# Optimization experiments

Hardware: AMD Instinct MI355X
Metric: run time of the kernel (lower is better)

## Reference

```python
import jax, jax.numpy as jnp
import numpy as np

EPS = 1e-12  # F.normalize default eps

def _l2norm(x, axis):
    n = jnp.sqrt(jnp.sum(x * x, axis=axis, keepdims=True))
    return x / jnp.maximum(n, EPS)

def setup_inputs() -> dict:
    key = jax.random.key(0)
    ks = jax.random.split(key, 6)
    N, C, K, B, OUT = 200000, 256, 64, 8, 1024
    alpha = 100.0
    feat = jax.random.normal(ks[0], (N, C), dtype=jnp.float32)
    batch_ids = jax.random.randint(ks[1], (N,), 0, B, dtype=jnp.int32)
    centroids = jax.random.uniform(ks[2], (K, C), dtype=jnp.float32)
    # _init_params: conv weight = 2*alpha*centroids, bias = -alpha*||centroid||_2
    conv_w = 2.0 * alpha * centroids
    conv_b = -alpha * jnp.sqrt(jnp.sum(centroids * centroids, axis=1))
    fc_w = jax.random.normal(ks[3], (OUT, K * C), dtype=jnp.float32) * (1.0 / np.sqrt(K * C))
    fc_b = jax.random.normal(ks[4], (OUT,), dtype=jnp.float32) * 0.01
    return {"feat": feat, "batch_ids": batch_ids, "centroids": centroids,
            "conv_w": conv_w, "conv_b": conv_b, "fc_w": fc_w, "fc_b": fc_b,
            "batch_size": B}

def reference(feat, batch_ids, centroids, conv_w, conv_b, fc_w, fc_b, batch_size):
    B = int(batch_size)
    K, C = centroids.shape
    # descriptor-wise L2 normalization (normalize_input=True)
    x = _l2norm(feat, axis=1)                       # [N, C]
    # 1x1 conv == linear: soft assignment logits per point
    logits = x @ conv_w.T + conv_b                  # [N, K]
    soft = jax.nn.softmax(logits, axis=1)           # [N, K]
    # Per-batch aggregation (replaces the python loop):
    # vlad[b,k,:] = sum_{p in b} soft[p,k] * x[p,:] - (sum_{p in b} soft[p,k]) * centroids[k,:]
    onehot = jax.nn.one_hot(batch_ids, B, dtype=x.dtype)          # [N, B]
    A = jnp.einsum('nb,nk,nc->bkc', onehot, soft, x)              # [B, K, C]
    S = jax.ops.segment_sum(soft, batch_ids, num_segments=B)      # [B, K]
    vlad = A - S[:, :, None] * centroids[None, :, :]              # [B, K, C]
    vlad = _l2norm(vlad, axis=2)                                  # intra-normalization over C
    v = vlad.reshape(B, K * C)
    out = v @ fc_w.T + fc_b                                       # [B, 1024]
    return _l2norm(out, axis=1)
```

## Files before the change

kernel.cpp:

```cpp
#include <hip/hip_runtime.h>
#include <hip/hip_bf16.h>

typedef __attribute__((ext_vector_type(8))) short bf16x8;
typedef __attribute__((ext_vector_type(4))) float f32x4;

#define PCAP 768

__global__ void p0_wsplit(const float* __restrict__ convw,
                          short* __restrict__ whi, short* __restrict__ wlo)
{
    int e = blockIdx.x * 256 + threadIdx.x;
    if (e >= 2048) return;
    int lane = e & 63;
    int kstep = (e >> 6) & 7;
    int nt = e >> 9;
    int cluster = nt * 16 + (lane & 15);
    int ch0 = kstep * 32 + (lane >> 4) * 8;
    const float* src = convw + cluster * 256 + ch0;
    #pragma unroll
    for (int j = 0; j < 8; ++j) {
        float x = src[j];
        unsigned u = __float_as_uint(x);
        unsigned uh = u & 0xffff0000u;
        float r = x - __uint_as_float(uh);
        whi[e * 8 + j] = (short)(u >> 16);
        wlo[e * 8 + j] = (short)(__float_as_uint(r) >> 16);
    }
}

__global__ __launch_bounds__(256) void p1_mfma(
    const float* __restrict__ feat, const int* __restrict__ bids,
    const short* __restrict__ whi, const short* __restrict__ wlo,
    const float* __restrict__ convb,
    float* __restrict__ soft, float* __restrict__ invn, int* __restrict__ cnts, int N)
{
    __shared__ float ssq_lds[64];
    __shared__ int cnt[8];
    const int t = threadIdx.x;
    if (t < 8) cnt[t] = 0;
    const int w = t >> 6, lane = t & 63;
    const int m = lane & 15, quad = lane >> 4;
    const int p0 = blockIdx.x * 64;
    const int gp = p0 + w * 16 + m;
    const bool valid = gp < N;

    f32x4 acc[4];
    #pragma unroll
    for (int nt = 0; nt < 4; ++nt) acc[nt] = (f32x4){0.f, 0.f, 0.f, 0.f};
    float ssq = 0.f;

    const float* frow = feat + (size_t)gp * 256 + quad * 8;
    const bf16x8* WH = (const bf16x8*)whi;
    const bf16x8* WL = (const bf16x8*)wlo;

    for (int ks = 0; ks < 8; ++ks) {
        float x[8];
        if (valid) {
            float4 v0 = *(const float4*)(frow + ks * 32);
            float4 v1 = *(const float4*)(frow + ks * 32 + 4);
            x[0] = v0.x; x[1] = v0.y; x[2] = v0.z; x[3] = v0.w;
            x[4] = v1.x; x[5] = v1.y; x[6] = v1.z; x[7] = v1.w;
        } else {
            #pragma unroll
            for (int j = 0; j < 8; ++j) x[j] = 0.f;
        }
        bf16x8 ahi, alo;
        #pragma unroll
        for (int j = 0; j < 8; ++j) {
            unsigned u = __float_as_uint(x[j]);
            unsigned uh = u & 0xffff0000u;
            float r = x[j] - __uint_as_float(uh);
            ahi[j] = (short)(u >> 16);
            alo[j] = (short)(__float_as_uint(r) >> 16);
            ssq += x[j] * x[j];
        }
        #pragma unroll
        for (int nt = 0; nt < 4; ++nt) {
            bf16x8 bhi = WH[(nt * 8 + ks) * 64 + lane];
            bf16x8 blo = WL[(nt * 8 + ks) * 64 + lane];
            acc[nt] = __builtin_amdgcn_mfma_f32_16x16x32_bf16(ahi, bhi, acc[nt], 0, 0, 0);
            acc[nt] = __builtin_amdgcn_mfma_f32_16x16x32_bf16(ahi, blo, acc[nt], 0, 0, 0);
            acc[nt] = __builtin_amdgcn_mfma_f32_16x16x32_bf16(alo, bhi, acc[nt], 0, 0, 0);
        }
    }

    ssq += __shfl_xor(ssq, 16);
    ssq += __shfl_xor(ssq, 32);
    if (quad == 0) ssq_lds[w * 16 + m] = ssq;
    __syncthreads();

    float bias[4];
    #pragma unroll
    for (int nt = 0; nt < 4; ++nt) bias[nt] = convb[nt * 16 + m];

    #pragma unroll
    for (int r = 0; r < 4; ++r) {
        int pl = quad * 4 + r;
        int gpt = p0 + w * 16 + pl;
        float inv = rsqrtf(fmaxf(ssq_lds[w * 16 + pl], 1e-24f));
        float v[4];
        #pragma unroll
        for (int nt = 0; nt < 4; ++nt) v[nt] = acc[nt][r] * inv + bias[nt];
        float mx = fmaxf(fmaxf(v[0], v[1]), fmaxf(v[2], v[3]));
        #pragma unroll
        for (int off = 8; off >= 1; off >>= 1) mx = fmaxf(mx, __shfl_xor(mx, off));
        float e[4];
        float s = 0.f;
        #pragma unroll
        for (int nt = 0; nt < 4; ++nt) { e[nt] = __expf(v[nt] - mx); s += e[nt]; }
        #pragma unroll
        for (int off = 8; off >= 1; off >>= 1) s += __shfl_xor(s, off);
        float rs = 1.0f / s;
        if (gpt < N) {
            #pragma unroll
            for (int nt = 0; nt < 4; ++nt)
                soft[(size_t)gpt * 64 + nt * 16 + m] = e[nt] * rs;
            if (m == 0) {
                invn[gpt] = inv;
                atomicAdd(&cnt[bids[gpt]], 1);
            }
        }
    }
    __syncthreads();
    if (t < 8) atomicAdd(&cnts[t], cnt[t]);
}

__global__ void p2_offsets(const int* __restrict__ cnts, int* __restrict__ offs, int* __restrict__ cur)
{
    if (threadIdx.x == 0) {
        int acc = 0;
        for (int b = 0; b < 8; ++b) { offs[b] = acc; cur[b] = acc; acc += cnts[b]; }
        offs[8] = acc;
    }
}

__global__ __launch_bounds__(256) void p2_scatter(
    const int* __restrict__ bids, int* __restrict__ cur, int* __restrict__ perm, int N)
{
    __shared__ int lcnt[8], lbase[8];
    const int t = threadIdx.x;
    if (t < 8) lcnt[t] = 0;
    __syncthreads();
    int p = blockIdx.x * 256 + t;
    int b = 0, my = 0;
    bool ok = p < N;
    if (ok) { b = bids[p]; my = atomicAdd(&lcnt[b], 1); }
    __syncthreads();
    if (t < 8) lbase[t] = atomicAdd(&cur[t], lcnt[t]);
    __syncthreads();
    if (ok) perm[lbase[b] + my] = p;
}

__global__ __launch_bounds__(256) void p3_mfma(
    const float* __restrict__ feat, const float* __restrict__ soft,
    const float* __restrict__ invn, const int* __restrict__ perm,
    const int* __restrict__ offs, float* __restrict__ partial,
    float* __restrict__ S, int split)
{
    __shared__ short xsT_hi[256 * 32];
    __shared__ short xsT_lo[256 * 32];
    __shared__ short sT_hi[64 * 32];
    __shared__ short sT_lo[64 * 32];
    __shared__ int   pidxL[PCAP];
    __shared__ float invL[PCAP];

    const int b  = blockIdx.x / split;
    const int sp = blockIdx.x % split;
    const int start = offs[b], end = offs[b + 1];
    const int len = end - start;
    const int chunk = (len + split - 1) / split;
    const int s0 = start + sp * chunk;
    int myLen = end - s0;
    myLen = max(0, min(myLen, chunk));
    myLen = min(myLen, PCAP);

    const int t = threadIdx.x;
    const int w = t >> 6, lane = t & 63;
    const int m = lane & 15, quad = lane >> 4;

    for (int i = t; i < myLen; i += 256) pidxL[i] = perm[s0 + i];
    __syncthreads();
    for (int i = t; i < myLen; i += 256) invL[i] = invn[pidxL[i]];
    __syncthreads();

    f32x4 acc[16];
    #pragma unroll
    for (int ct = 0; ct < 16; ++ct) acc[ct] = (f32x4){0.f, 0.f, 0.f, 0.f};
    float sacc = 0.f;

    const int nch = (myLen + 31) >> 5;
    for (int q = 0; q < nch; ++q) {
        const int p0 = q * 32;
        int pids[8];
        float pinv[8];
        #pragma unroll
        for (int j = 0; j < 8; ++j) {
            int pl = p0 + w * 8 + j;
            bool ok = pl < myLen;
            pids[j] = ok ? pidxL[pl] : -1;
            pinv[j] = ok ? invL[pl] : 0.f;
        }
        #pragma unroll
        for (int cg = 0; cg < 4; ++cg) {
            int c = cg * 64 + lane;
            float vals[8];
            #pragma unroll
            for (int j = 0; j < 8; ++j) {
                float v = 0.f;
                if (pids[j] >= 0) v = feat[(size_t)pids[j] * 256 + c] * pinv[j];
                vals[j] = v;
            }
            bf16x8 vh, vl;
            #pragma unroll
            for (int j = 0; j < 8; ++j) {
                unsigned u = __float_as_uint(vals[j]);
                float r = vals[j] - __uint_as_float(u & 0xffff0000u);
                vh[j] = (short)(u >> 16);
                vl[j] = (short)(__float_as_uint(r) >> 16);
            }
            *(bf16x8*)&xsT_hi[c * 32 + w * 8] = vh;
            *(bf16x8*)&xsT_lo[c * 32 + w * 8] = vl;
        }
        {
            float svals[8];
            #pragma unroll
            for (int j = 0; j < 8; ++j) {
                float v = 0.f;
                if (pids[j] >= 0) v = soft[(size_t)pids[j] * 64 + lane];
                svals[j] = v;
                sacc += v;
            }
            bf16x8 vh, vl;
            #pragma unroll
            for (int j = 0; j < 8; ++j) {
                unsigned u = __float_as_uint(svals[j]);
                float r = svals[j] - __uint_as_float(u & 0xffff0000u);
                vh[j] = (short)(u >> 16);
                vl[j] = (short)(__float_as_uint(r) >> 16);
            }
            *(bf16x8*)&sT_hi[lane * 32 + w * 8] = vh;
            *(bf16x8*)&sT_lo[lane * 32 + w * 8] = vl;
        }
        __syncthreads();
        bf16x8 ah = *(const bf16x8*)&sT_hi[(w * 16 + m) * 32 + quad * 8];
        bf16x8 al = *(const bf16x8*)&sT_lo[(w * 16 + m) * 32 + quad * 8];
        #pragma unroll
        for (int ct = 0; ct < 16; ++ct) {
            bf16x8 bh = *(const bf16x8*)&xsT_hi[(ct * 16 + m) * 32 + quad * 8];
            bf16x8 bl = *(const bf16x8*)&xsT_lo[(ct * 16 + m) * 32 + quad * 8];
            acc[ct] = __builtin_amdgcn_mfma_f32_16x16x32_bf16(ah, bh, acc[ct], 0, 0, 0);
            acc[ct] = __builtin_amdgcn_mfma_f32_16x16x32_bf16(ah, bl, acc[ct], 0, 0, 0);
            acc[ct] = __builtin_amdgcn_mfma_f32_16x16x32_bf16(al, bh, acc[ct], 0, 0, 0);
        }
        __syncthreads();
    }

    float* dst = partial + (size_t)(b * split + sp) * 64 * 256;
    #pragma unroll
    for (int ct = 0; ct < 16; ++ct) {
        #pragma unroll
        for (int r = 0; r < 4; ++r) {
            int k = w * 16 + quad * 4 + r;
            dst[k * 256 + ct * 16 + m] = acc[ct][r];
        }
    }
    atomicAdd(S + b * 64 + lane, sacc);
}

__global__ __launch_bounds__(256) void p4a_vlad(
    const float* __restrict__ partial, const float* __restrict__ S,
    const float* __restrict__ cents, float* __restrict__ v, int split)
{
    const int b = blockIdx.x >> 6, k = blockIdx.x & 63;
    const int t = threadIdx.x;
    float sum = 0.f;
    const float* base = partial + ((size_t)(b * split) * 64 + k) * 256 + t;
    for (int sp = 0; sp < split; ++sp)
        sum += base[(size_t)sp * 64 * 256];
    float val = sum - S[b * 64 + k] * cents[k * 256 + t];
    float sq = val * val;
    #pragma unroll
    for (int off = 32; off >= 1; off >>= 1) sq += __shfl_xor(sq, off);
    __shared__ float wsum[4];
    if ((t & 63) == 0) wsum[t >> 6] = sq;
    __syncthreads();
    float tot = wsum[0] + wsum[1] + wsum[2] + wsum[3];
    float r = 1.0f / fmaxf(sqrtf(tot), 1e-12f);
    v[b * 16384 + k * 256 + t] = val * r;
}

__global__ __launch_bounds__(256) void p4b_fc(
    const float* __restrict__ v, const float* __restrict__ fcw,
    const float* __restrict__ fcb, float* __restrict__ pre)
{
    const int t = threadIdx.x;
    const int o0 = blockIdx.x * 4;
    float acc[4][8] = {};
    for (int it = 0; it < 64; ++it) {
        int i = it * 256 + t;
        float wv[4];
        #pragma unroll
        for (int oo = 0; oo < 4; ++oo) wv[oo] = fcw[(size_t)(o0 + oo) * 16384 + i];
        #pragma unroll
        for (int b = 0; b < 8; ++b) {
            float vv = v[b * 16384 + i];
            #pragma unroll
            for (int oo = 0; oo < 4; ++oo) acc[oo][b] += wv[oo] * vv;
        }
    }
    __shared__ float red[32][4];
    #pragma unroll
    for (int oo = 0; oo < 4; ++oo)
        #pragma unroll
        for (int b = 0; b < 8; ++b) {
            float sv = acc[oo][b];
            #pragma unroll
            for (int off = 32; off >= 1; off >>= 1) sv += __shfl_xor(sv, off);
            if ((t & 63) == 0) red[oo * 8 + b][t >> 6] = sv;
        }
    __syncthreads();
    if (t < 32) {
        int oo = t >> 3, b = t & 7;
        float sv = red[t][0] + red[t][1] + red[t][2] + red[t][3];
        pre[b * 1024 + o0 + oo] = sv + fcb[o0 + oo];
    }
}

__global__ __launch_bounds__(256) void p5_norm(const float* __restrict__ pre, float* __restrict__ out)
{
    const int b = blockIdx.x, t = threadIdx.x;
    float vals[4];
    float sq = 0.f;
    #pragma unroll
    for (int i = 0; i < 4; ++i) {
        vals[i] = pre[b * 1024 + t + 256 * i];
        sq += vals[i] * vals[i];
    }
    #pragma unroll
    for (int off = 32; off >= 1; off >>= 1) sq += __shfl_xor(sq, off);
    __shared__ float wsum[4];
    if ((t & 63) == 0) wsum[t >> 6] = sq;
    __syncthreads();
    float tot = wsum[0] + wsum[1] + wsum[2] + wsum[3];
    float r = 1.0f / fmaxf(sqrtf(tot), 1e-12f);
    #pragma unroll
    for (int i = 0; i < 4; ++i) out[b * 1024 + t + 256 * i] = vals[i] * r;
}

extern "C" void kernel_launch(void* const* d_in, const int* in_sizes, int n_in,
                              void* d_out, int out_size, void* d_ws, size_t ws_size,
                              hipStream_t stream)
{
    const float* feat  = (const float*)d_in[0];
    const int*   bids  = (const int*)d_in[1];
    const float* cents = (const float*)d_in[2];
    const float* convw = (const float*)d_in[3];
    const float* convb = (const float*)d_in[4];
    const float* fcw   = (const float*)d_in[5];
    const float* fcb   = (const float*)d_in[6];
    float* out = (float*)d_out;

    const int N = in_sizes[0] / 256;

    const size_t base_floats = 16384
                             + (size_t)N * 64  + N
                             + 512  + 8 * 16384  + 8192 ;
    const size_t base_ints = (size_t)N + 8 + 9 + 8;
    int split = 96;
    while (split > 16) {
        size_t tot = (base_floats + (size_t)split * 8 * 16384) * 4 + base_ints * 4;
        if (tot <= ws_size) break;
        split -= 16;
    }

    short* whi = (short*)d_ws;
    short* wlo = whi + 16384;
    float* soft = (float*)(wlo + 16384);
    float* invn = soft + (size_t)N * 64;
    float* partial = invn + N;
    float* S    = partial + (size_t)split * 8 * 16384;
    float* v    = S + 512;
    float* pre  = v + 8 * 16384;
    int* perm = (int*)(pre + 8192);
    int* cnts = perm + N;
    int* offs = cnts + 8;
    int* cur  = offs + 9;

    hipMemsetAsync(S, 0, 512 * sizeof(float), stream);
    hipMemsetAsync(cnts, 0, 8 * sizeof(int), stream);

    p0_wsplit<<<8, 256, 0, stream>>>(convw, whi, wlo);
    p1_mfma<<<(N + 63) / 64, 256, 0, stream>>>(feat, bids, whi, wlo, convb, soft, invn, cnts, N);
    p2_offsets<<<1, 64, 0, stream>>>(cnts, offs, cur);
    p2_scatter<<<(N + 255) / 256, 256, 0, stream>>>(bids, cur, perm, N);
    p3_mfma<<<8 * split, 256, 0, stream>>>(feat, soft, invn, perm, offs, partial, S, split);
    p4a_vlad<<<512, 256, 0, stream>>>(partial, S, cents, v, split);
    p4b_fc<<<256, 256, 0, stream>>>(v, fcw, fcb, pre);
    p5_norm<<<8, 256, 0, stream>>>(pre, out);
}
```

Baseline: 582.5 us.

## Stage feature tiles into LDS via async global_load_lds with double buffering

The per-thread direct global loads of feature rows in the soft-assignment MFMA kernel are replaced by asynchronous global-to-LDS copies. The copies are double-buffered in 64-channel chunks with an XOR swizzle so the next chunk's load overlaps the current chunk's MFMAs. Weight fragments for each chunk are preloaded into registers, and the per-point norm is now shared with a lane shuffle rather than through LDS. The change uses 32 KB of LDS per block and adds a barrier per chunk, and the launch bound now requests 3 blocks per CU, which may limit occupancy or add register pressure.

```diff
diff --git a/kernel.cpp b/kernel.cpp
--- a/kernel.cpp
+++ b/kernel.cpp
@@ -5,6 +5,13 @@
 typedef __attribute__((ext_vector_type(4))) float f32x4;
 
 #define PCAP 768
+
+__device__ __forceinline__ void async_copy16(const void* g, void* l)
+{
+    __builtin_amdgcn_global_load_lds(
+        (const __attribute__((address_space(1))) unsigned int*)g,
+        (__attribute__((address_space(3))) unsigned int*)l, 16, 0, 0);
+}
 
 __global__ void p0_wsplit(const float* __restrict__ convw,
                           short* __restrict__ whi, short* __restrict__ wlo)
@@ -28,66 +35,94 @@
     }
 }
 
-__global__ __launch_bounds__(256) void p1_mfma(
+__global__ __launch_bounds__(256, 3) void p1_mfma(
     const float* __restrict__ feat, const int* __restrict__ bids,
     const short* __restrict__ whi, const short* __restrict__ wlo,
     const float* __restrict__ convb,
     float* __restrict__ soft, float* __restrict__ invn, int* __restrict__ cnts, int N)
 {
-    __shared__ float ssq_lds[64];
+    __shared__ float xbuf[2][4096];
     __shared__ int cnt[8];
     const int t = threadIdx.x;
     if (t < 8) cnt[t] = 0;
     const int w = t >> 6, lane = t & 63;
     const int m = lane & 15, quad = lane >> 4;
     const int p0 = blockIdx.x * 64;
-    const int gp = p0 + w * 16 + m;
-    const bool valid = gp < N;
+
+    int s_pt[4], s_inner[4];
+    #pragma unroll
+    for (int pass = 0; pass < 4; ++pass) {
+        int slot = pass * 256 + t;
+        s_pt[pass] = slot >> 4;
+        s_inner[pass] = (slot & 15) ^ (s_pt[pass] & 15);
+    }
+
+    auto STAGE = [&](int bi, int ck) {
+        #pragma unroll
+        for (int pass = 0; pass < 4; ++pass) {
+            int gpt = p0 + s_pt[pass];
+            const float* src = (gpt < N)
+                ? feat + (size_t)gpt * 256 + ck * 64 + s_inner[pass] * 4
+                : feat;
+            async_copy16(src, (char*)&xbuf[bi][0] + (size_t)(pass * 256 + w * 64) * 16);
+        }
+    };
+
+    STAGE(0, 0);
+    __syncthreads();
 
     f32x4 acc[4];
     #pragma unroll
     for (int nt = 0; nt < 4; ++nt) acc[nt] = (f32x4){0.f, 0.f, 0.f, 0.f};
     float ssq = 0.f;
 
-    const float* frow = feat + (size_t)gp * 256 + quad * 8;
     const bf16x8* WH = (const bf16x8*)whi;
     const bf16x8* WL = (const bf16x8*)wlo;
-
-    for (int ks = 0; ks < 8; ++ks) {
-        float x[8];
-        if (valid) {
-            float4 v0 = *(const float4*)(frow + ks * 32);
-            float4 v1 = *(const float4*)(frow + ks * 32 + 4);
-            x[0] = v0.x; x[1] = v0.y; x[2] = v0.z; x[3] = v0.w;
-            x[4] = v1.x; x[5] = v1.y; x[6] = v1.z; x[7] = v1.w;
-        } else {
-            #pragma unroll
-            for (int j = 0; j < 8; ++j) x[j] = 0.f;
-        }
-        bf16x8 ahi, alo;
-        #pragma unroll
-        for (int j = 0; j < 8; ++j) {
-            unsigned u = __float_as_uint(x[j]);
-            unsigned uh = u & 0xffff0000u;
-            float r = x[j] - __uint_as_float(uh);
-            ahi[j] = (short)(u >> 16);
-            alo[j] = (short)(__float_as_uint(r) >> 16);
-            ssq += x[j] * x[j];
-        }
-        #pragma unroll
-        for (int nt = 0; nt < 4; ++nt) {
-            bf16x8 bhi = WH[(nt * 8 + ks) * 64 + lane];
-            bf16x8 blo = WL[(nt * 8 + ks) * 64 + lane];
-            acc[nt] = __builtin_amdgcn_mfma_f32_16x16x32_bf16(ahi, bhi, acc[nt], 0, 0, 0);
-            acc[nt] = __builtin_amdgcn_mfma_f32_16x16x32_bf16(ahi, blo, acc[nt], 0, 0, 0);
-            acc[nt] = __builtin_amdgcn_mfma_f32_16x16x32_bf16(alo, bhi, acc[nt], 0, 0, 0);
-        }
+    const int ptl = w * 16 + m;
+
+    #pragma unroll
+    for (int ck = 0; ck < 4; ++ck) {
+        bf16x8 wfh[2][4], wfl[2][4];
+        #pragma unroll
+        for (int k2 = 0; k2 < 2; ++k2)
+            #pragma unroll
+            for (int nt = 0; nt < 4; ++nt) {
+                wfh[k2][nt] = WH[(nt * 8 + ck * 2 + k2) * 64 + lane];
+                wfl[k2][nt] = WL[(nt * 8 + ck * 2 + k2) * 64 + lane];
+            }
+        __builtin_amdgcn_sched_barrier(0);
+        if (ck < 3) STAGE((ck + 1) & 1, ck + 1);
+        __builtin_amdgcn_sched_barrier(0);
+
+        const float* B = &xbuf[ck & 1][0];
+        #pragma unroll
+        for (int k2 = 0; k2 < 2; ++k2) {
+            int i0 = (k2 * 8 + quad * 2 + 0) ^ m;
+            int i1 = (k2 * 8 + quad * 2 + 1) ^ m;
+            float4 v0 = *(const float4*)(B + (ptl * 16 + i0) * 4);
+            float4 v1 = *(const float4*)(B + (ptl * 16 + i1) * 4);
+            float x[8] = {v0.x, v0.y, v0.z, v0.w, v1.x, v1.y, v1.z, v1.w};
+            bf16x8 ahi, alo;
+            #pragma unroll
+            for (int j = 0; j < 8; ++j) {
+                unsigned u = __float_as_uint(x[j]);
+                float r = x[j] - __uint_as_float(u & 0xffff0000u);
+                ahi[j] = (short)(u >> 16);
+                alo[j] = (short)(__float_as_uint(r) >> 16);
+                ssq += x[j] * x[j];
+            }
+            #pragma unroll
+            for (int nt = 0; nt < 4; ++nt) {
+                acc[nt] = __builtin_amdgcn_mfma_f32_16x16x32_bf16(ahi, wfh[k2][nt], acc[nt], 0, 0, 0);
+                acc[nt] = __builtin_amdgcn_mfma_f32_16x16x32_bf16(ahi, wfl[k2][nt], acc[nt], 0, 0, 0);
+                acc[nt] = __builtin_amdgcn_mfma_f32_16x16x32_bf16(alo, wfh[k2][nt], acc[nt], 0, 0, 0);
+            }
+        }
+        if (ck < 3) __syncthreads();
     }
 
     ssq += __shfl_xor(ssq, 16);
     ssq += __shfl_xor(ssq, 32);
-    if (quad == 0) ssq_lds[w * 16 + m] = ssq;
-    __syncthreads();
 
     float bias[4];
     #pragma unroll
@@ -97,7 +132,8 @@
     for (int r = 0; r < 4; ++r) {
         int pl = quad * 4 + r;
         int gpt = p0 + w * 16 + pl;
-        float inv = rsqrtf(fmaxf(ssq_lds[w * 16 + pl], 1e-24f));
+        float sq = __shfl(ssq, pl);
+        float inv = rsqrtf(fmaxf(sq, 1e-24f));
         float v[4];
         #pragma unroll
         for (int nt = 0; nt < 4; ++nt) v[nt] = acc[nt][r] * inv + bias[nt];
```

After: 549.2 us. 1.06x faster.
